# Optimization experiments

Hardware: AMD Instinct MI355X
Metric: run time of the kernel (lower is better)

## Reference

```python
import jax, jax.numpy as jnp
import numpy as np

N_USERS = 1_000_000
N_GENDERS = 2
N_AGES = 8
EMBED_DIM = 32
N_NODES = 131072


def setup_inputs() -> dict:
    key = jax.random.key(0)
    k1, k2, k3, k4, k5, k6, k7, k8 = jax.random.split(key, 8)
    nodes = jax.random.randint(k1, (N_NODES,), 0, N_USERS)
    user_gender_list = jax.random.randint(k2, (N_USERS,), 0, N_GENDERS)
    user_age_list = jax.random.randint(k3, (N_USERS,), 0, N_AGES)
    u_emb = jax.random.normal(k4, (N_USERS, EMBED_DIM), dtype=jnp.float32) * 0.1
    g_emb = jax.random.normal(k5, (N_GENDERS, EMBED_DIM), dtype=jnp.float32) * 0.1
    a_emb = jax.random.normal(k6, (N_AGES, EMBED_DIM), dtype=jnp.float32) * 0.1
    # nn.Linear(3*embed_dim, embed_dim): weight [out, in], bias [out]
    lim = 1.0 / np.sqrt(3 * EMBED_DIM)
    W = jax.random.uniform(k7, (EMBED_DIM, 3 * EMBED_DIM), dtype=jnp.float32, minval=-lim, maxval=lim)
    b = jax.random.uniform(k8, (EMBED_DIM,), dtype=jnp.float32, minval=-lim, maxval=lim)
    return {
        "nodes": nodes,
        "user_gender_list": user_gender_list,
        "user_age_list": user_age_list,
        "u_emb": u_emb,
        "g_emb": g_emb,
        "a_emb": a_emb,
        "W": W,
        "b": b,
    }


def reference(nodes, user_gender_list, user_age_list, u_emb, g_emb, a_emb, W, b):
    # Single-neighbor attention: softmax over 1 element == 1.0 exactly,
    # so att_history == the embedding itself (degenerate attention).
    e_g = g_emb[user_gender_list[nodes]]   # [N, D]
    e_a = a_emb[user_age_list[nodes]]      # [N, D]
    e_u = u_emb[nodes]                     # [N, D]
    x = jnp.concatenate([e_g, e_a, e_u], axis=1)  # [N, 3D] (order: eg, ea, eu)
    return jax.nn.relu(x @ W.T + b)        # [N, D]
```

## Files before the change

kernel.cpp:

```cpp
#include <hip/hip_runtime.h>


#define NNODES   131072
#define BLOCK    256
#define SWS      68

typedef float floatx4 __attribute__((ext_vector_type(4)));

__global__ __launch_bounds__(BLOCK) void learnerc_agg_kernel(
    const int*   __restrict__ nodes,
    const int*   __restrict__ gender,
    const int*   __restrict__ age,
    const float* __restrict__ u_emb,
    const float* __restrict__ g_emb,
    const float* __restrict__ a_emb,
    const float* __restrict__ W,
    const float* __restrict__ b,
    float*       __restrict__ out)
{
    __shared__ float sW[32 * SWS];
    __shared__ float sGA[32 * 16];
    __shared__ float sG[64];
    __shared__ float sA[256];
    __shared__ float sB[32];

    const int t = threadIdx.x;
    const int n = blockIdx.x * BLOCK + t;

    const int node = nodes[n];
    const int g_of_n = gender[node];
    const int a_of_n = age[node];
    float u[32];
    {
        const float* up = u_emb + (size_t)node * 32;
        #pragma unroll
        for (int j = 0; j < 8; ++j) {
            const floatx4 v = *reinterpret_cast<const floatx4*>(up + j * 4);
            u[j * 4 + 0] = v.x; u[j * 4 + 1] = v.y;
            u[j * 4 + 2] = v.z; u[j * 4 + 3] = v.w;
        }
    }

    for (int c = t; c < 512; c += BLOCK) {
        const int d  = c >> 4;
        const int k4 = (c & 15) << 2;
        const floatx4 v = *reinterpret_cast<const floatx4*>(W + d * 96 + k4);
        *reinterpret_cast<floatx4*>(&sW[d * SWS + k4]) = v;
    }
    if (t < 64) sG[t] = g_emb[t];
    sA[t] = a_emb[t];
    if (t < 32) sB[t] = b[t];
    __syncthreads();

    for (int e = t; e < 512; e += BLOCK) {
        const int ga = e >> 5;
        const int d  = e & 31;
        const int g  = ga >> 3;
        const int aa = ga & 7;
        float acc = sB[d];
        #pragma unroll
        for (int k = 0; k < 32; ++k)
            acc += sG[g * 32 + k] * sW[d * SWS + k];
        #pragma unroll
        for (int k = 0; k < 32; ++k)
            acc += sA[aa * 32 + k] * sW[d * SWS + 32 + k];
        sGA[d * 16 + ga] = acc;
    }
    __syncthreads();

    const int ga = g_of_n * 8 + a_of_n;
    const float* Wu = W + 64;
    float* op = out + (size_t)n * 32;

    #pragma unroll
    for (int d4 = 0; d4 < 8; ++d4) {
        float rr[4];
        #pragma unroll
        for (int j = 0; j < 4; ++j) {
            const int d = d4 * 4 + j;
            float s = sGA[d * 16 + ga];
            #pragma unroll
            for (int k = 0; k < 32; ++k)
                s += u[k] * Wu[d * 96 + k];
            rr[j] = fmaxf(s, 0.0f);
        }
        floatx4 r; r.x = rr[0]; r.y = rr[1]; r.z = rr[2]; r.w = rr[3];
        __builtin_nontemporal_store(r, reinterpret_cast<floatx4*>(op + d4 * 4));
    }
}

extern "C" void kernel_launch(void* const* d_in, const int* in_sizes, int n_in,
                              void* d_out, int out_size, void* d_ws, size_t ws_size,
                              hipStream_t stream) {
    const int*   nodes  = (const int*)  d_in[0];
    const int*   gender = (const int*)  d_in[1];
    const int*   age    = (const int*)  d_in[2];
    const float* u_emb  = (const float*)d_in[3];
    const float* g_emb  = (const float*)d_in[4];
    const float* a_emb  = (const float*)d_in[5];
    const float* W      = (const float*)d_in[6];
    const float* b      = (const float*)d_in[7];
    float*       out    = (float*)d_out;

    const int grid = NNODES / BLOCK;
    learnerc_agg_kernel<<<grid, BLOCK, 0, stream>>>(
        nodes, gender, age, u_emb, g_emb, a_emb, W, b, out);
}
```

Measured before the change: 220.6 us.

## Precompute gender/age table in setup kernel and split output dims across threads

Adds a small setup kernel that computes the 16-entry gender/age projection table (bias included) and a transposed copy of the user-part weights into workspace. The main kernel now assigns four threads per node, each covering eight output dims, and handles two nodes per thread, reading the transposed weights from shared memory as vectors. This removes the per-block recomputation of the gender/age table and the uncached per-element global weight reads. The cost is an extra kernel launch, and output stores are now regular rather than nontemporal.

```diff
diff --git a/kernel.cpp b/kernel.cpp
--- a/kernel.cpp
+++ b/kernel.cpp
@@ -3,90 +3,133 @@
 
 #define NNODES   131072
 #define BLOCK    256
-#define SWS      68
+#define NPB      128
 
 typedef float floatx4 __attribute__((ext_vector_type(4)));
 
-__global__ __launch_bounds__(BLOCK) void learnerc_agg_kernel(
+__global__ __launch_bounds__(BLOCK) void learnerc_setup_kernel(
+    const float* __restrict__ g_emb,
+    const float* __restrict__ a_emb,
+    const float* __restrict__ W,
+    const float* __restrict__ b,
+    float*       __restrict__ ws)
+{
+    float* wuT = ws;
+    float* gaT = ws + 1024;
+    const int t = threadIdx.x;
+
+    if (blockIdx.x == 0) {
+        #pragma unroll
+        for (int c = t; c < 1024; c += BLOCK) {
+            const int d = c >> 5;
+            const int k = c & 31;
+            wuT[k * 32 + d] = W[d * 96 + 64 + k];
+        }
+    } else {
+        const int idx = (blockIdx.x - 1) * BLOCK + t;
+        const int ga  = idx >> 5;
+        const int d   = idx & 31;
+        const int g   = ga >> 3;
+        const int a   = ga & 7;
+        const float* wr = W + d * 96;
+        float acc = b[d];
+        #pragma unroll
+        for (int k = 0; k < 32; ++k) acc += g_emb[g * 32 + k] * wr[k];
+        #pragma unroll
+        for (int k = 0; k < 32; ++k) acc += a_emb[a * 32 + k] * wr[32 + k];
+        gaT[ga * 32 + d] = acc;
+    }
+}
+
+__global__ __launch_bounds__(BLOCK, 4) void learnerc_agg_kernel(
     const int*   __restrict__ nodes,
     const int*   __restrict__ gender,
     const int*   __restrict__ age,
     const float* __restrict__ u_emb,
-    const float* __restrict__ g_emb,
-    const float* __restrict__ a_emb,
-    const float* __restrict__ W,
-    const float* __restrict__ b,
+    const float* __restrict__ ws,
     float*       __restrict__ out)
 {
-    __shared__ float sW[32 * SWS];
-    __shared__ float sGA[32 * 16];
-    __shared__ float sG[64];
-    __shared__ float sA[256];
-    __shared__ float sB[32];
+    __shared__ float sWuT[1024];
 
-    const int t = threadIdx.x;
-    const int n = blockIdx.x * BLOCK + t;
+    const int t    = threadIdx.x;
+    const int dq   = t & 3;
+    const int slot = t >> 2;
+    const int n0   = blockIdx.x * NPB + slot;
+    const int n1   = n0 + 64;
 
-    const int node = nodes[n];
-    const int g_of_n = gender[node];
-    const int a_of_n = age[node];
-    float u[32];
+    const int node0 = nodes[n0];
+    const int node1 = nodes[n1];
+    const int gg0 = gender[node0], aa0 = age[node0];
+    const int gg1 = gender[node1], aa1 = age[node1];
+
+    float u0[32], u1[32];
     {
-        const float* up = u_emb + (size_t)node * 32;
+        const float* up0 = u_emb + (size_t)node0 * 32;
+        const float* up1 = u_emb + (size_t)node1 * 32;
         #pragma unroll
         for (int j = 0; j < 8; ++j) {
-            const floatx4 v = *reinterpret_cast<const floatx4*>(up + j * 4);
-            u[j * 4 + 0] = v.x; u[j * 4 + 1] = v.y;
-            u[j * 4 + 2] = v.z; u[j * 4 + 3] = v.w;
+            const floatx4 v = *reinterpret_cast<const floatx4*>(up0 + j * 4);
+            u0[j * 4 + 0] = v.x; u0[j * 4 + 1] = v.y;
+            u0[j * 4 + 2] = v.z; u0[j * 4 + 3] = v.w;
+        }
+        #pragma unroll
+        for (int j = 0; j < 8; ++j) {
+            const floatx4 v = *reinterpret_cast<const floatx4*>(up1 + j * 4);
+            u1[j * 4 + 0] = v.x; u1[j * 4 + 1] = v.y;
+            u1[j * 4 + 2] = v.z; u1[j * 4 + 3] = v.w;
         }
     }
 
-    for (int c = t; c < 512; c += BLOCK) {
-        const int d  = c >> 4;
-        const int k4 = (c & 15) << 2;
-        const floatx4 v = *reinterpret_cast<const floatx4*>(W + d * 96 + k4);
-        *reinterpret_cast<floatx4*>(&sW[d * SWS + k4]) = v;
-    }
-    if (t < 64) sG[t] = g_emb[t];
-    sA[t] = a_emb[t];
-    if (t < 32) sB[t] = b[t];
+    reinterpret_cast<floatx4*>(sWuT)[t] = reinterpret_cast<const floatx4*>(ws)[t];
     __syncthreads();
 
-    for (int e = t; e < 512; e += BLOCK) {
-        const int ga = e >> 5;
-        const int d  = e & 31;
-        const int g  = ga >> 3;
-        const int aa = ga & 7;
-        float acc = sB[d];
-        #pragma unroll
-        for (int k = 0; k < 32; ++k)
-            acc += sG[g * 32 + k] * sW[d * SWS + k];
-        #pragma unroll
-        for (int k = 0; k < 32; ++k)
-            acc += sA[aa * 32 + k] * sW[d * SWS + 32 + k];
-        sGA[d * 16 + ga] = acc;
+    const float* gaBase = ws + 1024;
+    float acc0[8], acc1[8];
+    {
+        const float* g0 = gaBase + (gg0 * 8 + aa0) * 32 + dq * 8;
+        const floatx4 c0 = *reinterpret_cast<const floatx4*>(g0);
+        const floatx4 c1 = *reinterpret_cast<const floatx4*>(g0 + 4);
+        acc0[0] = c0.x; acc0[1] = c0.y; acc0[2] = c0.z; acc0[3] = c0.w;
+        acc0[4] = c1.x; acc0[5] = c1.y; acc0[6] = c1.z; acc0[7] = c1.w;
+        const float* g1 = gaBase + (gg1 * 8 + aa1) * 32 + dq * 8;
+        const floatx4 d0 = *reinterpret_cast<const floatx4*>(g1);
+        const floatx4 d1 = *reinterpret_cast<const floatx4*>(g1 + 4);
+        acc1[0] = d0.x; acc1[1] = d0.y; acc1[2] = d0.z; acc1[3] = d0.w;
+        acc1[4] = d1.x; acc1[5] = d1.y; acc1[6] = d1.z; acc1[7] = d1.w;
     }
-    __syncthreads();
 
-    const int ga = g_of_n * 8 + a_of_n;
-    const float* Wu = W + 64;
-    float* op = out + (size_t)n * 32;
+    const float* wbase = sWuT + dq * 8;
+    #pragma unroll
+    for (int k = 0; k < 32; ++k) {
+        const floatx4 wlo = *reinterpret_cast<const floatx4*>(wbase + k * 32);
+        const floatx4 whi = *reinterpret_cast<const floatx4*>(wbase + k * 32 + 4);
+        const float uk0 = u0[k];
+        const float uk1 = u1[k];
+        acc0[0] += uk0 * wlo.x; acc0[1] += uk0 * wlo.y;
+        acc0[2] += uk0 * wlo.z; acc0[3] += uk0 * wlo.w;
+        acc0[4] += uk0 * whi.x; acc0[5] += uk0 * whi.y;
+        acc0[6] += uk0 * whi.z; acc0[7] += uk0 * whi.w;
+        acc1[0] += uk1 * wlo.x; acc1[1] += uk1 * wlo.y;
+        acc1[2] += uk1 * wlo.z; acc1[3] += uk1 * wlo.w;
+        acc1[4] += uk1 * whi.x; acc1[5] += uk1 * whi.y;
+        acc1[6] += uk1 * whi.z; acc1[7] += uk1 * whi.w;
+    }
 
-    #pragma unroll
-    for (int d4 = 0; d4 < 8; ++d4) {
-        float rr[4];
-        #pragma unroll
-        for (int j = 0; j < 4; ++j) {
-            const int d = d4 * 4 + j;
-            float s = sGA[d * 16 + ga];
-            #pragma unroll
-            for (int k = 0; k < 32; ++k)
-                s += u[k] * Wu[d * 96 + k];
-            rr[j] = fmaxf(s, 0.0f);
-        }
-        floatx4 r; r.x = rr[0]; r.y = rr[1]; r.z = rr[2]; r.w = rr[3];
-        __builtin_nontemporal_store(r, reinterpret_cast<floatx4*>(op + d4 * 4));
-    }
+    float* op0 = out + (size_t)n0 * 32 + dq * 8;
+    float* op1 = out + (size_t)n1 * 32 + dq * 8;
+    floatx4 r;
+    r.x = fmaxf(acc0[0], 0.f); r.y = fmaxf(acc0[1], 0.f);
+    r.z = fmaxf(acc0[2], 0.f); r.w = fmaxf(acc0[3], 0.f);
+    *reinterpret_cast<floatx4*>(op0) = r;
+    r.x = fmaxf(acc0[4], 0.f); r.y = fmaxf(acc0[5], 0.f);
+    r.z = fmaxf(acc0[6], 0.f); r.w = fmaxf(acc0[7], 0.f);
+    *reinterpret_cast<floatx4*>(op0 + 4) = r;
+    r.x = fmaxf(acc1[0], 0.f); r.y = fmaxf(acc1[1], 0.f);
+    r.z = fmaxf(acc1[2], 0.f); r.w = fmaxf(acc1[3], 0.f);
+    *reinterpret_cast<floatx4*>(op1) = r;
+    r.x = fmaxf(acc1[4], 0.f); r.y = fmaxf(acc1[5], 0.f);
+    r.z = fmaxf(acc1[6], 0.f); r.w = fmaxf(acc1[7], 0.f);
+    *reinterpret_cast<floatx4*>(op1 + 4) = r;
 }
 
 extern "C" void kernel_launch(void* const* d_in, const int* in_sizes, int n_in,
@@ -101,8 +144,11 @@
     const float* W      = (const float*)d_in[6];
     const float* b      = (const float*)d_in[7];
     float*       out    = (float*)d_out;
+    float*       ws     = (float*)d_ws;
 
-    const int grid = NNODES / BLOCK;
+    learnerc_setup_kernel<<<3, BLOCK, 0, stream>>>(g_emb, a_emb, W, b, ws);
+
+    const int grid = NNODES / NPB;
     learnerc_agg_kernel<<<grid, BLOCK, 0, stream>>>(
-        nodes, gender, age, u_emb, g_emb, a_emb, W, b, out);
+        nodes, gender, age, u_emb, ws, out);
 }
```

Result: faster. 196.8 us (-10.8%).
